# Optimization experiments

Hardware: AMD Instinct MI355X
Metric: run time of the kernel (lower is better)

## Reference

```python
import jax, jax.numpy as jnp
import numpy as np

B, T, D, H = 256, 512, 128, 128  # batch, seq_len, input feat, hidden


def setup_inputs() -> dict:
    key = jax.random.key(0)
    ks = jax.random.split(key, 7)
    s_in = 1.0 / np.sqrt(D)
    s_h = 1.0 / np.sqrt(H)
    return {
        "x": jax.random.normal(ks[0], (B, T, D), dtype=jnp.float32),
        # layer 0: kernel [D, 3H], recurrent kernel [H, 3H], bias [2, 3H] (reset_after=True)
        "W0": jax.random.uniform(ks[1], (D, 3 * H), jnp.float32, -s_in, s_in),
        "U0": jax.random.uniform(ks[2], (H, 3 * H), jnp.float32, -s_h, s_h),
        "b0": jnp.zeros((2, 3 * H), jnp.float32),
        # layer 1: input dim = H
        "W1": jax.random.uniform(ks[3], (H, 3 * H), jnp.float32, -s_h, s_h),
        "U1": jax.random.uniform(ks[4], (H, 3 * H), jnp.float32, -s_h, s_h),
        "b1": jnp.zeros((2, 3 * H), jnp.float32),
    }


def _gru_layer(x, W, U, b):
    """Keras GRU (reset_after=True), return_sequences=True, eval mode (no dropout).
    x: [B, T, D]; W: [D, 3H]; U: [H, 3H]; b: [2, 3H]. Gate order: z, r, h.
    """
    b_in, b_rec = b[0], b[1]
    # precompute input projection for all timesteps: [B, T, 3H]
    xp = jnp.einsum("btd,dg->btg", x, W) + b_in
    h0 = jnp.zeros((x.shape[0], U.shape[0]), x.dtype)

    def step(h, xt):
        rec = h @ U + b_rec                       # [B, 3H]
        xz, xr, xh = jnp.split(xt, 3, axis=-1)
        rz, rr, rh = jnp.split(rec, 3, axis=-1)
        z = jax.nn.sigmoid(xz + rz)
        r = jax.nn.sigmoid(xr + rr)
        hh = jnp.tanh(xh + r * rh)                # reset applied after recurrent matmul
        h_new = z * h + (1.0 - z) * hh
        return h_new, h_new

    _, ys = jax.lax.scan(step, h0, jnp.swapaxes(xp, 0, 1))  # [T, B, H]
    return jnp.swapaxes(ys, 0, 1)                            # [B, T, H]


def reference(x, W0, U0, b0, W1, U1, b1):
    h = _gru_layer(x, W0, U0, b0)
    h = _gru_layer(h, W1, U1, b1)
    return h
```

## Files before the change

### kernel.cpp

```cpp
#include <hip/hip_runtime.h>
#include <cstdint>
#include <cstddef>

typedef __bf16 bf16x8 __attribute__((ext_vector_type(8)));
typedef __bf16 bf16x4 __attribute__((ext_vector_type(4)));
typedef float  f32x4  __attribute__((ext_vector_type(4)));

#define MFMA16(a,b,c) __builtin_amdgcn_mfma_f32_16x16x32_bf16((a),(b),(c),0,0,0)

#define BAR_LGKM() __asm__ volatile("s_waitcnt lgkmcnt(0)\n\ts_barrier" ::: "memory")
#define BAR_FULL() __asm__ volatile("s_waitcnt vmcnt(0) lgkmcnt(0)\n\ts_barrier" ::: "memory")

#define L2E  1.4426950408889634f
#define L2E2 2.8853900817779268f


__global__ void prep_frags(const float* __restrict__ W0, const float* __restrict__ U0,
                           const float* __restrict__ W1, const float* __restrict__ U1,
                           __bf16* __restrict__ frags, int* __restrict__ flags)
{
    if (blockIdx.x == 0 && threadIdx.x < 16) flags[threadIdx.x * 16] = 0;
    int id = blockIdx.x * 512 + threadIdx.x;
    int layer = id / 12288;
    int r     = id % 12288;
    int lane = r & 63;
    int ctkt = r >> 6;
    int kt = ctkt & 7;
    int ct = ctkt >> 3;
    const float* Wsrc = layer ? W1 : W0;
    const float* Usrc = layer ? U1 : U0;
    int n  = ct * 16 + (lane & 15);
    int k0 = kt * 32 + (lane >> 4) * 8;
    const float* src = (k0 < 128) ? (Wsrc + (size_t)k0 * 384)
                                  : (Usrc + (size_t)(k0 - 128) * 384);
    const float s = (ct < 16) ? L2E : L2E2;
    __bf16* dst = frags + (size_t)layer * 98304 + (size_t)r * 8;
#pragma unroll
    for (int j = 0; j < 8; j++)
        dst[j] = (__bf16)(src[(size_t)j * 384 + n] * s);
}

__global__ __launch_bounds__(512, 2) void gru_pipe(
    const float* x, const __bf16* __restrict__ frags,
    const float* __restrict__ b0, const float* __restrict__ b1,
    float* h0, float* out, int* flags)
{
    __shared__ __align__(16) __bf16 ab[2][16 * 264];

    const int tid  = threadIdx.x;
    const int wave = tid >> 6, lane = tid & 63;
    const int l15  = lane & 15, quad = lane >> 4;
    const int pair  = blockIdx.x & 15;
    const int layer = blockIdx.x >> 4;
    const int B0 = pair * 16;
    int* const flagp = flags + pair * 16;

    const __bf16* Bf  = frags + (size_t)layer * 98304;
    const float* bias = layer ? b1 : b0;
    const float* xin  = layer ? h0 : x;
    float*       hout = layer ? out : h0;

    bf16x8 bfr[3][8];
#pragma unroll
    for (int g = 0; g < 3; g++) {
        int ct = 8 * g + wave;
#pragma unroll
        for (int kt = 0; kt < 8; kt++) {
            bfr[g][kt] = *(const bf16x8*)(Bf + (size_t)((ct * 8 + kt) * 64 + lane) * 8);
            __asm__ volatile("" : "+v"(bfr[g][kt]));
        }
    }

    const int j = wave * 16 + l15;
    const float bz  = (bias[j]       + bias[384 + j]) * L2E;
    const float br  = (bias[128 + j] + bias[512 + j]) * L2E;
    const float bxh = bias[256 + j] * L2E2;
    const float brh = bias[640 + j] * L2E2;

    const int srow = tid >> 5;
    const int c4   = (tid & 31) * 4;
    const float* px = xin + (size_t)(B0 + srow) * 65536 + c4;
    const int sidx = srow * 264 + c4;

    const size_t obase = (size_t)(B0 + quad * 4) * 65536 + j;

    int known = 0;
    if (layer) {
        while (known < 2) {
            __builtin_amdgcn_s_sleep(4);
            known = __hip_atomic_load(flagp, __ATOMIC_RELAXED,
                                      __HIP_MEMORY_SCOPE_AGENT);
        }
    }

    f32x4 vc = layer ? __builtin_nontemporal_load((const f32x4*)px)
                     : *(const f32x4*)px;
    {
        bf16x4 hv;
        hv.x = (__bf16)vc[0]; hv.y = (__bf16)vc[1];
        hv.z = (__bf16)vc[2]; hv.w = (__bf16)vc[3];
        *(bf16x4*)&ab[0][sidx] = hv;
    }
    if (tid < 256) {
        int row = tid >> 4, seg = tid & 15;
        *(uint4*)&ab[0][row * 264 + 128 + seg * 8] = make_uint4(0, 0, 0, 0);
    }
    __syncthreads();
    vc = layer ? __builtin_nontemporal_load((const f32x4*)(px + 128))
               : *(const f32x4*)(px + 128);

    float hold[4] = {0.f, 0.f, 0.f, 0.f};
    const int abase = l15 * 264 + quad * 8;

    for (int t = 0; t < 512; t++) {
        const int cur = t & 1, nxt = cur ^ 1;

        if (layer) {
            int need = t + 3; if (need > 512) need = 512;
            while (known < need) {
                __builtin_amdgcn_s_sleep(4);
                known = __hip_atomic_load(flagp, __ATOMIC_RELAXED,
                                          __HIP_MEMORY_SCOPE_AGENT);
            }
        }
        const int t2 = (t < 510) ? (t + 2) : 511;
        f32x4 vn = layer
            ? __builtin_nontemporal_load((const f32x4*)(px + (size_t)t2 * 128))
            : *(const f32x4*)(px + (size_t)t2 * 128);

        bf16x8 A[8];
#pragma unroll
        for (int kt = 0; kt < 8; kt++)
            A[kt] = *(const bf16x8*)&ab[cur][abase + kt * 32];

        f32x4 acc[4] = {{0,0,0,0},{0,0,0,0},{0,0,0,0},{0,0,0,0}};
        __builtin_amdgcn_s_setprio(1);
#pragma unroll
        for (int kt = 0; kt < 8; kt++) {
            acc[0] = MFMA16(A[kt], bfr[0][kt], acc[0]);
            acc[1] = MFMA16(A[kt], bfr[1][kt], acc[1]);
            acc[(kt < 4) ? 2 : 3] = MFMA16(A[kt], bfr[2][kt], acc[(kt < 4) ? 2 : 3]);
        }
        __builtin_amdgcn_s_setprio(0);

        float hnew[4];
#pragma unroll
        for (int r = 0; r < 4; r++) {
            float z  = __builtin_amdgcn_rcpf(
                           1.f + __builtin_amdgcn_exp2f(-(acc[0][r] + bz)));
            float rg = __builtin_amdgcn_rcpf(
                           1.f + __builtin_amdgcn_exp2f(-(acc[1][r] + br)));
            float hp = (acc[2][r] + bxh) + rg * (acc[3][r] + brh);
            float e2 = __builtin_amdgcn_exp2f(hp);
            float th = 1.f - 2.f * __builtin_amdgcn_rcpf(e2 + 1.f);
            hnew[r] = th + z * (hold[r] - th);
            hold[r] = hnew[r];
        }

        {
            bf16x4 hv;
            hv.x = (__bf16)vc[0]; hv.y = (__bf16)vc[1];
            hv.z = (__bf16)vc[2]; hv.w = (__bf16)vc[3];
            *(bf16x4*)&ab[nxt][sidx] = hv;
        }
#pragma unroll
        for (int r = 0; r < 4; r++)
            ab[nxt][(quad * 4 + r) * 264 + 128 + j] = (__bf16)hnew[r];

        if (layer == 0 && (t & 3) == 3) {
            BAR_FULL();
            if (tid == 0)
                __hip_atomic_store(flagp, t, __ATOMIC_RELAXED,
                                   __HIP_MEMORY_SCOPE_AGENT);
        } else {
            BAR_LGKM();
        }

        if (layer == 0) {
#pragma unroll
            for (int r = 0; r < 4; r++)
                __builtin_nontemporal_store(hnew[r],
                    hout + obase + (size_t)r * 65536 + (size_t)t * 128);
        } else {
#pragma unroll
            for (int r = 0; r < 4; r++)
                hout[obase + (size_t)r * 65536 + (size_t)t * 128] = hnew[r];
        }

        vc = vn;
    }

    if (layer == 0) {
        BAR_FULL();
        if (tid == 0)
            __hip_atomic_store(flagp, 512, __ATOMIC_RELAXED,
                               __HIP_MEMORY_SCOPE_AGENT);
    }
}

extern "C" void kernel_launch(void* const* d_in, const int* in_sizes, int n_in,
                              void* d_out, int out_size, void* d_ws, size_t ws_size,
                              hipStream_t stream)
{
    const float* x  = (const float*)d_in[0];
    const float* W0 = (const float*)d_in[1];
    const float* U0 = (const float*)d_in[2];
    const float* b0 = (const float*)d_in[3];
    const float* W1 = (const float*)d_in[4];
    const float* U1 = (const float*)d_in[5];
    const float* b1 = (const float*)d_in[6];
    float* out = (float*)d_out;

    char* ws = (char*)d_ws;
    __bf16* frags = (__bf16*)ws;
    int*    flags = (int*)(ws + 393216);
    float* h0;
    const size_t need = 458752 + 67108864;
    if (ws_size >= need) h0 = (float*)(ws + 458752);
    else                 h0 = out;

    prep_frags<<<48, 512, 0, stream>>>(W0, U0, W1, U1, frags, flags);
    gru_pipe<<<32, 512, 0, stream>>>(x, frags, b0, b1, h0, out, flags);
}
```

Measured before the change: 576.1 us.

## Software-pipeline input projection ahead of the recurrent matmul with swizzled LDS

Splits the per-step GEMM into recurrent (h@U) and input (x@W) parts. The input projection for step t+2 is computed after the recurrent MFMAs of step t, which shortens the serial dependency chain that runs through h. The loop is unrolled by two so the even and odd precomputed accumulators stay in registers. The LDS buffers are split into separate x and h buffers with an XOR swizzle in place of padding. Prefetch depth and the layer-1 flag lookahead are raised, at the cost of more registers and more complex indexing.

```diff
diff --git a/kernel.cpp b/kernel.cpp
--- a/kernel.cpp
+++ b/kernel.cpp
@@ -45,7 +45,8 @@
     const float* __restrict__ b0, const float* __restrict__ b1,
     float* h0, float* out, int* flags)
 {
-    __shared__ __align__(16) __bf16 ab[2][16 * 264];
+    __shared__ __align__(16) __bf16 xb[2][2048];
+    __shared__ __align__(16) __bf16 hb[2][2048];
 
     const int tid  = threadIdx.x;
     const int wave = tid >> 6, lane = tid & 63;
@@ -60,14 +61,16 @@
     const float* xin  = layer ? h0 : x;
     float*       hout = layer ? out : h0;
 
-    bf16x8 bfr[3][8];
+    bf16x8 bw[3][4], bu[3][4];
 #pragma unroll
     for (int g = 0; g < 3; g++) {
         int ct = 8 * g + wave;
 #pragma unroll
-        for (int kt = 0; kt < 8; kt++) {
-            bfr[g][kt] = *(const bf16x8*)(Bf + (size_t)((ct * 8 + kt) * 64 + lane) * 8);
-            __asm__ volatile("" : "+v"(bfr[g][kt]));
+        for (int kt = 0; kt < 4; kt++) {
+            bw[g][kt] = *(const bf16x8*)(Bf + (size_t)((ct * 8 + kt) * 64 + lane) * 8);
+            bu[g][kt] = *(const bf16x8*)(Bf + (size_t)((ct * 8 + kt + 4) * 64 + lane) * 8);
+            __asm__ volatile("" : "+v"(bw[g][kt]));
+            __asm__ volatile("" : "+v"(bu[g][kt]));
         }
     }
 
@@ -78,117 +81,172 @@
     const float brh = bias[640 + j] * L2E2;
 
     const int srow = tid >> 5;
-    const int c4   = (tid & 31) * 4;
-    const float* px = xin + (size_t)(B0 + srow) * 65536 + c4;
-    const int sidx = srow * 264 + c4;
+    const float* px = xin + (size_t)(B0 + srow) * 65536 + (tid & 31) * 4;
+    const int sb = (srow * 256 + (tid & 31) * 8) ^ ((srow & 7) << 4);
+
+    const int swz = (l15 & 7) << 4;
+    const int abb = l15 * 256 + quad * 16;
+    const int ao0 = (abb      ) ^ swz;
+    const int ao1 = (abb +  64) ^ swz;
+    const int ao2 = (abb + 128) ^ swz;
+    const int ao3 = (abb + 192) ^ swz;
+    int hw_[4];
+#pragma unroll
+    for (int r = 0; r < 4; r++) {
+        int row = quad * 4 + r;
+        hw_[r] = (row * 256 + j * 2) ^ ((row & 7) << 4);
+    }
 
     const size_t obase = (size_t)(B0 + quad * 4) * 65536 + j;
 
     int known = 0;
     if (layer) {
-        while (known < 2) {
+        while (known < 4) {
             __builtin_amdgcn_s_sleep(4);
             known = __hip_atomic_load(flagp, __ATOMIC_RELAXED,
                                       __HIP_MEMORY_SCOPE_AGENT);
         }
     }
 
-    f32x4 vc = layer ? __builtin_nontemporal_load((const f32x4*)px)
-                     : *(const f32x4*)px;
-    {
-        bf16x4 hv;
-        hv.x = (__bf16)vc[0]; hv.y = (__bf16)vc[1];
-        hv.z = (__bf16)vc[2]; hv.w = (__bf16)vc[3];
-        *(bf16x4*)&ab[0][sidx] = hv;
-    }
-    if (tid < 256) {
-        int row = tid >> 4, seg = tid & 15;
-        *(uint4*)&ab[0][row * 264 + 128 + seg * 8] = make_uint4(0, 0, 0, 0);
+#define LOADX(p) (layer ? __builtin_nontemporal_load((const f32x4*)(p)) \
+                        : *(const f32x4*)(p))
+#define PACKST(buf, v) do { bf16x4 hv_;                                  \
+        hv_.x = (__bf16)(v)[0]; hv_.y = (__bf16)(v)[1];                  \
+        hv_.z = (__bf16)(v)[2]; hv_.w = (__bf16)(v)[3];                  \
+        *(bf16x4*)((char*)&(buf)[0] + sb) = hv_; } while (0)
+
+    const f32x4 zv = {0.f, 0.f, 0.f, 0.f};
+
+    {
+        f32x4 v0 = LOADX(px);
+        f32x4 v1 = LOADX(px + 128);
+        PACKST(xb[0], v0);
+        PACKST(xb[1], v1);
+        ((uint64_t*)&hb[0][0])[tid] = 0ull;
     }
     __syncthreads();
-    vc = layer ? __builtin_nontemporal_load((const f32x4*)(px + 128))
-               : *(const f32x4*)(px + 128);
-
+
+    f32x4 xpzE = zv, xprE = zv, xphE = zv;
+    f32x4 xpzO = zv, xprO = zv, xphO = zv;
+    {
+        bf16x8 Ax0 = *(const bf16x8*)((const char*)&xb[0][0] + ao0);
+        bf16x8 Ax1 = *(const bf16x8*)((const char*)&xb[0][0] + ao1);
+        bf16x8 Ax2 = *(const bf16x8*)((const char*)&xb[0][0] + ao2);
+        bf16x8 Ax3 = *(const bf16x8*)((const char*)&xb[0][0] + ao3);
+        xpzE = MFMA16(Ax0, bw[0][0], xpzE); xprE = MFMA16(Ax0, bw[1][0], xprE); xphE = MFMA16(Ax0, bw[2][0], xphE);
+        xpzE = MFMA16(Ax1, bw[0][1], xpzE); xprE = MFMA16(Ax1, bw[1][1], xprE); xphE = MFMA16(Ax1, bw[2][1], xphE);
+        xpzE = MFMA16(Ax2, bw[0][2], xpzE); xprE = MFMA16(Ax2, bw[1][2], xprE); xphE = MFMA16(Ax2, bw[2][2], xphE);
+        xpzE = MFMA16(Ax3, bw[0][3], xpzE); xprE = MFMA16(Ax3, bw[1][3], xprE); xphE = MFMA16(Ax3, bw[2][3], xphE);
+    }
+    {
+        bf16x8 Ax0 = *(const bf16x8*)((const char*)&xb[1][0] + ao0);
+        bf16x8 Ax1 = *(const bf16x8*)((const char*)&xb[1][0] + ao1);
+        bf16x8 Ax2 = *(const bf16x8*)((const char*)&xb[1][0] + ao2);
+        bf16x8 Ax3 = *(const bf16x8*)((const char*)&xb[1][0] + ao3);
+        xpzO = MFMA16(Ax0, bw[0][0], xpzO); xprO = MFMA16(Ax0, bw[1][0], xprO); xphO = MFMA16(Ax0, bw[2][0], xphO);
+        xpzO = MFMA16(Ax1, bw[0][1], xpzO); xprO = MFMA16(Ax1, bw[1][1], xprO); xphO = MFMA16(Ax1, bw[2][1], xphO);
+        xpzO = MFMA16(Ax2, bw[0][2], xpzO); xprO = MFMA16(Ax2, bw[1][2], xprO); xphO = MFMA16(Ax2, bw[2][2], xphO);
+        xpzO = MFMA16(Ax3, bw[0][3], xpzO); xprO = MFMA16(Ax3, bw[1][3], xprO); xphO = MFMA16(Ax3, bw[2][3], xphO);
+    }
+    __syncthreads();
+    {
+        f32x4 v2 = LOADX(px + 256);
+        PACKST(xb[0], v2);
+    }
+    f32x4 vc = LOADX(px + 384);
     float hold[4] = {0.f, 0.f, 0.f, 0.f};
-    const int abase = l15 * 264 + quad * 8;
-
-    for (int t = 0; t < 512; t++) {
-        const int cur = t & 1, nxt = cur ^ 1;
-
-        if (layer) {
-            int need = t + 3; if (need > 512) need = 512;
-            while (known < need) {
-                __builtin_amdgcn_s_sleep(4);
-                known = __hip_atomic_load(flagp, __ATOMIC_RELAXED,
-                                          __HIP_MEMORY_SCOPE_AGENT);
-            }
-        }
-        const int t2 = (t < 510) ? (t + 2) : 511;
-        f32x4 vn = layer
-            ? __builtin_nontemporal_load((const f32x4*)(px + (size_t)t2 * 128))
-            : *(const f32x4*)(px + (size_t)t2 * 128);
-
-        bf16x8 A[8];
-#pragma unroll
-        for (int kt = 0; kt < 8; kt++)
-            A[kt] = *(const bf16x8*)&ab[cur][abase + kt * 32];
-
-        f32x4 acc[4] = {{0,0,0,0},{0,0,0,0},{0,0,0,0},{0,0,0,0}};
-        __builtin_amdgcn_s_setprio(1);
-#pragma unroll
-        for (int kt = 0; kt < 8; kt++) {
-            acc[0] = MFMA16(A[kt], bfr[0][kt], acc[0]);
-            acc[1] = MFMA16(A[kt], bfr[1][kt], acc[1]);
-            acc[(kt < 4) ? 2 : 3] = MFMA16(A[kt], bfr[2][kt], acc[(kt < 4) ? 2 : 3]);
-        }
-        __builtin_amdgcn_s_setprio(0);
-
-        float hnew[4];
-#pragma unroll
-        for (int r = 0; r < 4; r++) {
-            float z  = __builtin_amdgcn_rcpf(
-                           1.f + __builtin_amdgcn_exp2f(-(acc[0][r] + bz)));
-            float rg = __builtin_amdgcn_rcpf(
-                           1.f + __builtin_amdgcn_exp2f(-(acc[1][r] + br)));
-            float hp = (acc[2][r] + bxh) + rg * (acc[3][r] + brh);
-            float e2 = __builtin_amdgcn_exp2f(hp);
-            float th = 1.f - 2.f * __builtin_amdgcn_rcpf(e2 + 1.f);
-            hnew[r] = th + z * (hold[r] - th);
-            hold[r] = hnew[r];
-        }
-
-        {
-            bf16x4 hv;
-            hv.x = (__bf16)vc[0]; hv.y = (__bf16)vc[1];
-            hv.z = (__bf16)vc[2]; hv.w = (__bf16)vc[3];
-            *(bf16x4*)&ab[nxt][sidx] = hv;
-        }
-#pragma unroll
-        for (int r = 0; r < 4; r++)
-            ab[nxt][(quad * 4 + r) * 264 + 128 + j] = (__bf16)hnew[r];
-
-        if (layer == 0 && (t & 3) == 3) {
-            BAR_FULL();
-            if (tid == 0)
-                __hip_atomic_store(flagp, t, __ATOMIC_RELAXED,
-                                   __HIP_MEMORY_SCOPE_AGENT);
-        } else {
-            BAR_LGKM();
-        }
-
-        if (layer == 0) {
-#pragma unroll
-            for (int r = 0; r < 4; r++)
-                __builtin_nontemporal_store(hnew[r],
-                    hout + obase + (size_t)r * 65536 + (size_t)t * 128);
-        } else {
-#pragma unroll
-            for (int r = 0; r < 4; r++)
-                hout[obase + (size_t)r * 65536 + (size_t)t * 128] = hnew[r];
-        }
-
-        vc = vn;
-    }
+    __syncthreads();
+
+#define GRU_BODY(T, S, xpz, xpr, xph)                                         \
+    {                                                                         \
+        const int t_ = (T);                                                   \
+        if (layer) {                                  \
+            int need = t_ + 5; if (need > 512) need = 512;                    \
+            while (known < need) {                                            \
+                __builtin_amdgcn_s_sleep(4);                                  \
+                known = __hip_atomic_load(flagp, __ATOMIC_RELAXED,            \
+                                          __HIP_MEMORY_SCOPE_AGENT);          \
+            }                                                                 \
+        }                                                                     \
+        int t4_ = t_ + 4; if (t4_ > 511) t4_ = 511;                           \
+        f32x4 vn = LOADX(px + (size_t)t4_ * 128);                             \
+        bf16x8 Ah0 = *(const bf16x8*)((const char*)&hb[S][0] + ao0);          \
+        bf16x8 Ah1 = *(const bf16x8*)((const char*)&hb[S][0] + ao1);          \
+        bf16x8 Ah2 = *(const bf16x8*)((const char*)&hb[S][0] + ao2);          \
+        bf16x8 Ah3 = *(const bf16x8*)((const char*)&hb[S][0] + ao3);          \
+        f32x4 az = xpz, ar = xpr, ahh = zv;                                   \
+        __builtin_amdgcn_s_setprio(1);                                        \
+        az = MFMA16(Ah0, bu[0][0], az); ar = MFMA16(Ah0, bu[1][0], ar);       \
+        ahh = MFMA16(Ah0, bu[2][0], ahh);                                     \
+        az = MFMA16(Ah1, bu[0][1], az); ar = MFMA16(Ah1, bu[1][1], ar);       \
+        ahh = MFMA16(Ah1, bu[2][1], ahh);                                     \
+        az = MFMA16(Ah2, bu[0][2], az); ar = MFMA16(Ah2, bu[1][2], ar);       \
+        ahh = MFMA16(Ah2, bu[2][2], ahh);                                     \
+        az = MFMA16(Ah3, bu[0][3], az); ar = MFMA16(Ah3, bu[1][3], ar);       \
+        ahh = MFMA16(Ah3, bu[2][3], ahh);                                     \
+            \
+        bf16x8 Ax0 = *(const bf16x8*)((const char*)&xb[S][0] + ao0);          \
+        bf16x8 Ax1 = *(const bf16x8*)((const char*)&xb[S][0] + ao1);          \
+        bf16x8 Ax2 = *(const bf16x8*)((const char*)&xb[S][0] + ao2);          \
+        bf16x8 Ax3 = *(const bf16x8*)((const char*)&xb[S][0] + ao3);          \
+        f32x4 xhc = xph;                             \
+        xpz = zv; xpr = zv; xph = zv;                                         \
+        xpz = MFMA16(Ax0, bw[0][0], xpz); xpr = MFMA16(Ax0, bw[1][0], xpr);   \
+        xph = MFMA16(Ax0, bw[2][0], xph);                                     \
+        xpz = MFMA16(Ax1, bw[0][1], xpz); xpr = MFMA16(Ax1, bw[1][1], xpr);   \
+        xph = MFMA16(Ax1, bw[2][1], xph);                                     \
+        xpz = MFMA16(Ax2, bw[0][2], xpz); xpr = MFMA16(Ax2, bw[1][2], xpr);   \
+        xph = MFMA16(Ax2, bw[2][2], xph);                                     \
+        xpz = MFMA16(Ax3, bw[0][3], xpz); xpr = MFMA16(Ax3, bw[1][3], xpr);   \
+        xph = MFMA16(Ax3, bw[2][3], xph);                                     \
+        __builtin_amdgcn_s_setprio(0);                                        \
+                        \
+        float hnew[4];                                                        \
+        _Pragma("unroll")                                                     \
+        for (int r = 0; r < 4; r++) {                                         \
+            float z  = __builtin_amdgcn_rcpf(                                 \
+                           1.f + __builtin_amdgcn_exp2f(-(az[r] + bz)));      \
+            float rg = __builtin_amdgcn_rcpf(                                 \
+                           1.f + __builtin_amdgcn_exp2f(-(ar[r] + br)));      \
+            float hp = (xhc[r] + bxh) + rg * (ahh[r] + brh);                  \
+            float e2 = __builtin_amdgcn_exp2f(hp);                            \
+            float th = 1.f - 2.f * __builtin_amdgcn_rcpf(e2 + 1.f);           \
+            hnew[r] = th + z * (hold[r] - th);                                \
+            hold[r] = hnew[r];                                                \
+        }                                                                     \
+                         \
+        PACKST(xb[(S) ^ 1], vc);                                              \
+        _Pragma("unroll")                                                     \
+        for (int r = 0; r < 4; r++)                                           \
+            *(__bf16*)((char*)&hb[(S) ^ 1][0] + hw_[r]) = (__bf16)hnew[r];    \
+        if (layer == 0 && (t_ & 3) == 3) {                                    \
+            BAR_FULL();                 \
+            if (tid == 0)                                                     \
+                __hip_atomic_store(flagp, t_, __ATOMIC_RELAXED,               \
+                                   __HIP_MEMORY_SCOPE_AGENT);                 \
+        } else {                                                              \
+            BAR_LGKM();                                                       \
+        }                                                                     \
+        if (layer == 0) {                                                     \
+            _Pragma("unroll")                                                 \
+            for (int r = 0; r < 4; r++)                                       \
+                __builtin_nontemporal_store(hnew[r],                          \
+                    hout + obase + (size_t)r * 65536 + (size_t)t_ * 128);     \
+        } else {                                                              \
+            _Pragma("unroll")                                                 \
+            for (int r = 0; r < 4; r++)                                       \
+                hout[obase + (size_t)r * 65536 + (size_t)t_ * 128] = hnew[r]; \
+        }                                                                     \
+        vc = vn;                                                              \
+    }
+
+    for (int it = 0; it < 256; ++it) {
+        GRU_BODY(2 * it,     0, xpzE, xprE, xphE);
+        GRU_BODY(2 * it + 1, 1, xpzO, xprO, xphO);
+    }
+#undef GRU_BODY
+#undef PACKST
+#undef LOADX
 
     if (layer == 0) {
         BAR_FULL();
```

Measured after the change: 552.5 us. 1.04x faster.

## Split workgroup into input-projection and recurrent wave groups with pipelined partials

Applied to the files above, without the earlier changes.

Doubles the workgroup to 16 waves. Eight waves compute the input projection for the next timestep and write partial gate sums to shared memory. The other eight waves perform only the recurrent half-K MFMAs plus the gate math. This takes the input-projection MFMAs off the serial critical path of each timestep, and the LDS layout is XOR-swizzled to reduce bank conflicts. The cost is extra LDS traffic for the fp32 partials, a barrier shared by both wave groups, and a prefetch distance that grows by one step.

```diff
diff --git a/kernel.cpp b/kernel.cpp
--- a/kernel.cpp
+++ b/kernel.cpp
@@ -40,16 +40,20 @@
         dst[j] = (__bf16)(src[(size_t)j * 384 + n] * s);
 }
 
-__global__ __launch_bounds__(512, 2) void gru_pipe(
+__global__ __launch_bounds__(1024, 4) void gru_pipe(
     const float* x, const __bf16* __restrict__ frags,
     const float* __restrict__ b0, const float* __restrict__ b1,
     float* h0, float* out, int* flags)
 {
-    __shared__ __align__(16) __bf16 ab[2][16 * 264];
+    __shared__ __align__(16) __bf16 xb[2][2048];
+    __shared__ __align__(16) __bf16 hb[2][2048];
+    __shared__ __align__(16) float  pp[2][6144];
 
     const int tid  = threadIdx.x;
     const int wave = tid >> 6, lane = tid & 63;
     const int l15  = lane & 15, quad = lane >> 4;
+    const bool is_xp = (wave < 8);
+    const int  w8   = wave & 7;
     const int pair  = blockIdx.x & 15;
     const int layer = blockIdx.x >> 4;
     const int B0 = pair * 16;
@@ -60,142 +64,188 @@
     const float* xin  = layer ? h0 : x;
     float*       hout = layer ? out : h0;
 
-    bf16x8 bfr[3][8];
+    const int ktoff = is_xp ? 0 : 4;
+    bf16x8 bf_[3][4];
 #pragma unroll
     for (int g = 0; g < 3; g++) {
-        int ct = 8 * g + wave;
-#pragma unroll
-        for (int kt = 0; kt < 8; kt++) {
-            bfr[g][kt] = *(const bf16x8*)(Bf + (size_t)((ct * 8 + kt) * 64 + lane) * 8);
-            __asm__ volatile("" : "+v"(bfr[g][kt]));
+        int ct = 8 * g + w8;
+#pragma unroll
+        for (int kt = 0; kt < 4; kt++) {
+            bf_[g][kt] = *(const bf16x8*)(Bf + (size_t)((ct * 8 + kt + ktoff) * 64 + lane) * 8);
+            __asm__ volatile("" : "+v"(bf_[g][kt]));
         }
     }
 
-    const int j = wave * 16 + l15;
+    const int j = w8 * 16 + l15;
     const float bz  = (bias[j]       + bias[384 + j]) * L2E;
     const float br  = (bias[128 + j] + bias[512 + j]) * L2E;
     const float bxh = bias[256 + j] * L2E2;
     const float brh = bias[640 + j] * L2E2;
 
     const int srow = tid >> 5;
-    const int c4   = (tid & 31) * 4;
-    const float* px = xin + (size_t)(B0 + srow) * 65536 + c4;
-    const int sidx = srow * 264 + c4;
+    const float* px = xin + (size_t)(B0 + (srow & 15)) * 65536 + (tid & 31) * 4;
+    const int sb = ((srow & 15) * 256 + (tid & 31) * 8) ^ ((srow & 7) << 4);
+
+    const int swz = (l15 & 7) << 4;
+    const int abb = l15 * 256 + quad * 16;
+    const int ao0 = (abb      ) ^ swz;
+    const int ao1 = (abb +  64) ^ swz;
+    const int ao2 = (abb + 128) ^ swz;
+    const int ao3 = (abb + 192) ^ swz;
+    int hw_[4];
+#pragma unroll
+    for (int r = 0; r < 4; r++) {
+        int row = quad * 4 + r;
+        hw_[r] = (row * 256 + j * 2) ^ ((row & 7) << 4);
+    }
+    const int ppo = w8 * 256 + lane * 4;
 
     const size_t obase = (size_t)(B0 + quad * 4) * 65536 + j;
 
+#define LOADX(p) (layer ? __builtin_nontemporal_load((const f32x4*)(p)) \
+                        : *(const f32x4*)(p))
+#define PACKST(buf, v) do { bf16x4 hv_;                                  \
+        hv_.x = (__bf16)(v)[0]; hv_.y = (__bf16)(v)[1];                  \
+        hv_.z = (__bf16)(v)[2]; hv_.w = (__bf16)(v)[3];                  \
+        *(bf16x4*)((char*)&(buf)[0] + sb) = hv_; } while (0)
+
+    const f32x4 zv = {0.f, 0.f, 0.f, 0.f};
+    f32x4 vc = zv;
     int known = 0;
-    if (layer) {
-        while (known < 2) {
+
+    if (layer && is_xp) {
+        while (known < 3) {
             __builtin_amdgcn_s_sleep(4);
             known = __hip_atomic_load(flagp, __ATOMIC_RELAXED,
                                       __HIP_MEMORY_SCOPE_AGENT);
         }
     }
-
-    f32x4 vc = layer ? __builtin_nontemporal_load((const f32x4*)px)
-                     : *(const f32x4*)px;
-    {
-        bf16x4 hv;
-        hv.x = (__bf16)vc[0]; hv.y = (__bf16)vc[1];
-        hv.z = (__bf16)vc[2]; hv.w = (__bf16)vc[3];
-        *(bf16x4*)&ab[0][sidx] = hv;
-    }
-    if (tid < 256) {
-        int row = tid >> 4, seg = tid & 15;
-        *(uint4*)&ab[0][row * 264 + 128 + seg * 8] = make_uint4(0, 0, 0, 0);
+    if (is_xp) {
+        f32x4 v0 = LOADX(px);
+        PACKST(xb[0], v0);
+    } else {
+        ((uint64_t*)&hb[0][0])[tid & 511] = 0ull;
     }
     __syncthreads();
-    vc = layer ? __builtin_nontemporal_load((const f32x4*)(px + 128))
-               : *(const f32x4*)(px + 128);
-
+    if (is_xp) {
+        bf16x8 A0 = *(const bf16x8*)((const char*)&xb[0][0] + ao0);
+        bf16x8 A1 = *(const bf16x8*)((const char*)&xb[0][0] + ao1);
+        bf16x8 A2 = *(const bf16x8*)((const char*)&xb[0][0] + ao2);
+        bf16x8 A3 = *(const bf16x8*)((const char*)&xb[0][0] + ao3);
+        f32x4 cz = zv, cr = zv, ch = zv;
+        cz = MFMA16(A0, bf_[0][0], cz); cr = MFMA16(A0, bf_[1][0], cr); ch = MFMA16(A0, bf_[2][0], ch);
+        cz = MFMA16(A1, bf_[0][1], cz); cr = MFMA16(A1, bf_[1][1], cr); ch = MFMA16(A1, bf_[2][1], ch);
+        cz = MFMA16(A2, bf_[0][2], cz); cr = MFMA16(A2, bf_[1][2], cr); ch = MFMA16(A2, bf_[2][2], ch);
+        cz = MFMA16(A3, bf_[0][3], cz); cr = MFMA16(A3, bf_[1][3], cr); ch = MFMA16(A3, bf_[2][3], ch);
+        *(f32x4*)&pp[0][ppo]        = cz;
+        *(f32x4*)&pp[0][2048 + ppo] = cr;
+        *(f32x4*)&pp[0][4096 + ppo] = ch;
+    }
+    BAR_LGKM();
+    if (is_xp) {
+        f32x4 v1 = LOADX(px + 128);
+        PACKST(xb[0], v1);
+        vc = LOADX(px + 256);
+    }
     float hold[4] = {0.f, 0.f, 0.f, 0.f};
-    const int abase = l15 * 264 + quad * 8;
-
-    for (int t = 0; t < 512; t++) {
+    BAR_LGKM();
+
+    for (int t = 0; t < 512; ++t) {
         const int cur = t & 1, nxt = cur ^ 1;
 
-        if (layer) {
-            int need = t + 3; if (need > 512) need = 512;
-            while (known < need) {
-                __builtin_amdgcn_s_sleep(4);
-                known = __hip_atomic_load(flagp, __ATOMIC_RELAXED,
-                                          __HIP_MEMORY_SCOPE_AGENT);
-            }
-        }
-        const int t2 = (t < 510) ? (t + 2) : 511;
-        f32x4 vn = layer
-            ? __builtin_nontemporal_load((const f32x4*)(px + (size_t)t2 * 128))
-            : *(const f32x4*)(px + (size_t)t2 * 128);
-
-        bf16x8 A[8];
-#pragma unroll
-        for (int kt = 0; kt < 8; kt++)
-            A[kt] = *(const bf16x8*)&ab[cur][abase + kt * 32];
-
-        f32x4 acc[4] = {{0,0,0,0},{0,0,0,0},{0,0,0,0},{0,0,0,0}};
-        __builtin_amdgcn_s_setprio(1);
-#pragma unroll
-        for (int kt = 0; kt < 8; kt++) {
-            acc[0] = MFMA16(A[kt], bfr[0][kt], acc[0]);
-            acc[1] = MFMA16(A[kt], bfr[1][kt], acc[1]);
-            acc[(kt < 4) ? 2 : 3] = MFMA16(A[kt], bfr[2][kt], acc[(kt < 4) ? 2 : 3]);
-        }
-        __builtin_amdgcn_s_setprio(0);
-
-        float hnew[4];
-#pragma unroll
-        for (int r = 0; r < 4; r++) {
-            float z  = __builtin_amdgcn_rcpf(
-                           1.f + __builtin_amdgcn_exp2f(-(acc[0][r] + bz)));
-            float rg = __builtin_amdgcn_rcpf(
-                           1.f + __builtin_amdgcn_exp2f(-(acc[1][r] + br)));
-            float hp = (acc[2][r] + bxh) + rg * (acc[3][r] + brh);
-            float e2 = __builtin_amdgcn_exp2f(hp);
-            float th = 1.f - 2.f * __builtin_amdgcn_rcpf(e2 + 1.f);
-            hnew[r] = th + z * (hold[r] - th);
-            hold[r] = hnew[r];
-        }
-
-        {
-            bf16x4 hv;
-            hv.x = (__bf16)vc[0]; hv.y = (__bf16)vc[1];
-            hv.z = (__bf16)vc[2]; hv.w = (__bf16)vc[3];
-            *(bf16x4*)&ab[nxt][sidx] = hv;
-        }
-#pragma unroll
-        for (int r = 0; r < 4; r++)
-            ab[nxt][(quad * 4 + r) * 264 + 128 + j] = (__bf16)hnew[r];
-
-        if (layer == 0 && (t & 3) == 3) {
-            BAR_FULL();
-            if (tid == 0)
+        if (is_xp) {
+            if (layer) {
+                int need = t + 4; if (need > 512) need = 512;
+                while (known < need) {
+                    __builtin_amdgcn_s_sleep(4);
+                    known = __hip_atomic_load(flagp, __ATOMIC_RELAXED,
+                                              __HIP_MEMORY_SCOPE_AGENT);
+                }
+            }
+            const int t3 = (t < 509) ? (t + 3) : 511;
+            f32x4 vn = LOADX(px + (size_t)t3 * 128);
+
+            bf16x8 A0 = *(const bf16x8*)((const char*)&xb[cur][0] + ao0);
+            bf16x8 A1 = *(const bf16x8*)((const char*)&xb[cur][0] + ao1);
+            bf16x8 A2 = *(const bf16x8*)((const char*)&xb[cur][0] + ao2);
+            bf16x8 A3 = *(const bf16x8*)((const char*)&xb[cur][0] + ao3);
+            f32x4 cz = zv, cr = zv, ch = zv;
+            cz = MFMA16(A0, bf_[0][0], cz); cr = MFMA16(A0, bf_[1][0], cr); ch = MFMA16(A0, bf_[2][0], ch);
+            cz = MFMA16(A1, bf_[0][1], cz); cr = MFMA16(A1, bf_[1][1], cr); ch = MFMA16(A1, bf_[2][1], ch);
+            cz = MFMA16(A2, bf_[0][2], cz); cr = MFMA16(A2, bf_[1][2], cr); ch = MFMA16(A2, bf_[2][2], ch);
+            cz = MFMA16(A3, bf_[0][3], cz); cr = MFMA16(A3, bf_[1][3], cr); ch = MFMA16(A3, bf_[2][3], ch);
+            *(f32x4*)&pp[nxt][ppo]        = cz;
+            *(f32x4*)&pp[nxt][2048 + ppo] = cr;
+            *(f32x4*)&pp[nxt][4096 + ppo] = ch;
+
+            PACKST(xb[nxt], vc);
+            vc = vn;
+
+            BAR_LGKM();
+            if (layer == 0 && (t & 3) == 3 && tid == 0)
                 __hip_atomic_store(flagp, t, __ATOMIC_RELAXED,
                                    __HIP_MEMORY_SCOPE_AGENT);
         } else {
-            BAR_LGKM();
+            bf16x8 A0 = *(const bf16x8*)((const char*)&hb[cur][0] + ao0);
+            bf16x8 A1 = *(const bf16x8*)((const char*)&hb[cur][0] + ao1);
+            bf16x8 A2 = *(const bf16x8*)((const char*)&hb[cur][0] + ao2);
+            bf16x8 A3 = *(const bf16x8*)((const char*)&hb[cur][0] + ao3);
+            f32x4 az  = *(const f32x4*)&pp[cur][ppo];
+            f32x4 ar  = *(const f32x4*)&pp[cur][2048 + ppo];
+            f32x4 xh  = *(const f32x4*)&pp[cur][4096 + ppo];
+            f32x4 ahh = zv;
+            __builtin_amdgcn_s_setprio(1);
+            az = MFMA16(A0, bf_[0][0], az); ar = MFMA16(A0, bf_[1][0], ar); ahh = MFMA16(A0, bf_[2][0], ahh);
+            az = MFMA16(A1, bf_[0][1], az); ar = MFMA16(A1, bf_[1][1], ar); ahh = MFMA16(A1, bf_[2][1], ahh);
+            az = MFMA16(A2, bf_[0][2], az); ar = MFMA16(A2, bf_[1][2], ar); ahh = MFMA16(A2, bf_[2][2], ahh);
+            az = MFMA16(A3, bf_[0][3], az); ar = MFMA16(A3, bf_[1][3], ar); ahh = MFMA16(A3, bf_[2][3], ahh);
+            __builtin_amdgcn_s_setprio(0);
+
+            float hnew[4];
+#pragma unroll
+            for (int r = 0; r < 4; r++) {
+                float z  = __builtin_amdgcn_rcpf(
+                               1.f + __builtin_amdgcn_exp2f(-(az[r] + bz)));
+                float rg = __builtin_amdgcn_rcpf(
+                               1.f + __builtin_amdgcn_exp2f(-(ar[r] + br)));
+                float hp = (xh[r] + bxh) + rg * (ahh[r] + brh);
+                float e2 = __builtin_amdgcn_exp2f(hp);
+                float th = 1.f - 2.f * __builtin_amdgcn_rcpf(e2 + 1.f);
+                hnew[r] = th + z * (hold[r] - th);
+                hold[r] = hnew[r];
+            }
+
+#pragma unroll
+            for (int r = 0; r < 4; r++)
+                *(__bf16*)((char*)&hb[nxt][0] + hw_[r]) = (__bf16)hnew[r];
+
+            if (layer == 0 && (t & 3) == 3) {
+                BAR_FULL();
+            } else {
+                BAR_LGKM();
+            }
+
+            if (layer == 0) {
+#pragma unroll
+                for (int r = 0; r < 4; r++)
+                    __builtin_nontemporal_store(hnew[r],
+                        hout + obase + (size_t)r * 65536 + (size_t)t * 128);
+            } else {
+#pragma unroll
+                for (int r = 0; r < 4; r++)
+                    hout[obase + (size_t)r * 65536 + (size_t)t * 128] = hnew[r];
+            }
         }
-
-        if (layer == 0) {
-#pragma unroll
-            for (int r = 0; r < 4; r++)
-                __builtin_nontemporal_store(hnew[r],
-                    hout + obase + (size_t)r * 65536 + (size_t)t * 128);
-        } else {
-#pragma unroll
-            for (int r = 0; r < 4; r++)
-                hout[obase + (size_t)r * 65536 + (size_t)t * 128] = hnew[r];
-        }
-
-        vc = vn;
     }
 
     if (layer == 0) {
-        BAR_FULL();
+        if (is_xp) { BAR_LGKM(); } else { BAR_FULL(); }
         if (tid == 0)
             __hip_atomic_store(flagp, 512, __ATOMIC_RELAXED,
                                __HIP_MEMORY_SCOPE_AGENT);
     }
+#undef PACKST
+#undef LOADX
 }
 
 extern "C" void kernel_launch(void* const* d_in, const int* in_sizes, int n_in,
@@ -220,5 +270,5 @@
     else                 h0 = out;
 
     prep_frags<<<48, 512, 0, stream>>>(W0, U0, W1, U1, frags, flags);
-    gru_pipe<<<32, 512, 0, stream>>>(x, frags, b0, b1, h0, out, flags);
+    gru_pipe<<<32, 1024, 0, stream>>>(x, frags, b0, b1, h0, out, flags);
 }
```

After: 598.5 us. +3.9%, slower.
